# Kernel tuning notes

Measured on AMD Instinct MI355X. Metric: run time of the kernel, lower is better.

## Reference

```python
import jax, jax.numpy as jnp
import numpy as np

N = 20000      # nodes
E = 320000     # edges
F = 32         # node_feat_dim
H = 128        # hidden_dim
HEADS = 4
DH = 128       # out_channels per head (PyG TransformerConv semantics)
L = 2          # number of GNNBlocks actually built


def _ln(x, s, b, eps=1e-5):
    m = x.mean(-1, keepdims=True)
    v = ((x - m) ** 2).mean(-1, keepdims=True)
    return (x - m) / jnp.sqrt(v + eps) * s + b


def setup_inputs() -> dict:
    key = jax.random.key(0)
    ks = jax.random.split(key, 16)
    nrm = lambda k, sh, sc=0.05: jax.random.normal(k, sh, dtype=jnp.float32) * sc
    inp = {}
    inp['x'] = jax.random.normal(ks[0], (N, F), dtype=jnp.float32)
    inp['edge_index'] = jax.random.randint(ks[1], (2, E), 0, N)
    inp['Win'] = nrm(ks[2], (F, H))
    inp['b_in'] = jnp.zeros((H,), jnp.float32)
    inp['ln1_s'] = jnp.ones((L, H), jnp.float32)
    inp['ln1_b'] = jnp.zeros((L, H), jnp.float32)
    inp['Wq'] = nrm(ks[3], (L, H, HEADS * DH))
    inp['bq'] = jnp.zeros((L, HEADS * DH), jnp.float32)
    inp['Wk'] = nrm(ks[4], (L, H, HEADS * DH))
    inp['bk'] = jnp.zeros((L, HEADS * DH), jnp.float32)
    inp['Wv'] = nrm(ks[5], (L, H, HEADS * DH))
    inp['bv'] = jnp.zeros((L, HEADS * DH), jnp.float32)
    inp['Wskip'] = nrm(ks[6], (L, H, H))
    inp['bskip'] = jnp.zeros((L, H), jnp.float32)
    inp['Wbeta'] = nrm(ks[7], (L, 3 * H, 1))
    inp['ln2_s'] = jnp.ones((L, H), jnp.float32)
    inp['ln2_b'] = jnp.zeros((L, H), jnp.float32)
    inp['W1'] = nrm(ks[8], (L, H, 4 * H))
    inp['b1'] = jnp.zeros((L, 4 * H), jnp.float32)
    inp['W2'] = nrm(ks[9], (L, 4 * H, H))
    inp['b2'] = jnp.zeros((L, H), jnp.float32)
    inp['g1'] = jnp.ones((L,), jnp.float32)
    inp['g2'] = jnp.ones((L,), jnp.float32)
    inp['lno_s'] = jnp.ones((H,), jnp.float32)
    inp['lno_b'] = jnp.zeros((H,), jnp.float32)
    return inp


def reference(x, edge_index, Win, b_in, ln1_s, ln1_b, Wq, bq, Wk, bk, Wv, bv,
              Wskip, bskip, Wbeta, ln2_s, ln2_b, W1, b1, W2, b2, g1, g2,
              lno_s, lno_b):
    src, dst = edge_index[0], edge_index[1]  # messages flow src -> dst
    n = x.shape[0]
    scale = 1.0 / np.sqrt(DH).astype(np.float32)
    h = x @ Win + b_in  # [N,H]
    for l in range(L):
        # --- pre-norm TransformerConv (heads=4, concat=False, beta=True) ---
        hn = _ln(h, ln1_s[l], ln1_b[l])
        q = (hn @ Wq[l] + bq[l]).reshape(n, HEADS, DH)
        k = (hn @ Wk[l] + bk[l]).reshape(n, HEADS, DH)
        v = (hn @ Wv[l] + bv[l]).reshape(n, HEADS, DH)
        # per-edge attention logits [E, HEADS]
        alpha = jnp.einsum('ehd,ehd->eh', q[dst], k[src]) * scale
        # segment softmax over incoming edges of each target node
        amax = jax.ops.segment_max(alpha, dst, num_segments=n)  # [N,HEADS]
        num = jnp.exp(alpha - amax[dst])
        den = jax.ops.segment_sum(num, dst, num_segments=n)      # [N,HEADS]
        a = num / den[dst]                                       # [E,HEADS]
        # scatter-aggregate weighted values, then mean over heads (concat=False)
        agg = jax.ops.segment_sum(a[:, :, None] * v[src], dst, num_segments=n)
        out = agg.mean(axis=1)                                   # [N,H]
        # root skip + beta gate
        xr = hn @ Wskip[l] + bskip[l]
        beta = jax.nn.sigmoid(
            jnp.concatenate([out, xr, out - xr], axis=-1) @ Wbeta[l])  # [N,1]
        attn = beta * xr + (1.0 - beta) * out
        h = h + g1[l] * attn
        # --- pre-norm FFN ---
        hn2 = _ln(h, ln2_s[l], ln2_b[l])
        ffn = jax.nn.gelu(hn2 @ W1[l] + b1[l], approximate=False) @ W2[l] + b2[l]
        h = h + g2[l] * ffn
    return _ln(h, lno_s, lno_b)
```

## Files before the change

### kernel.cpp

```cpp
#include <hip/hip_runtime.h>
#include <hip/hip_bf16.h>
#include <math.h>

#define NN 20000
#define NE 320000

typedef unsigned short ushort_t;
typedef unsigned short ushortx8 __attribute__((ext_vector_type(8)));
typedef short s16x8 __attribute__((ext_vector_type(8)));
typedef float f32x4 __attribute__((ext_vector_type(4)));
typedef float f32x2 __attribute__((ext_vector_type(2)));

__device__ __forceinline__ float us2f(unsigned short u){
  return __uint_as_float(((unsigned)u) << 16);
}
__device__ __forceinline__ unsigned short f2us(float f){
  unsigned u = __float_as_uint(f);
  unsigned r = (u + 0x7fffu + ((u >> 16) & 1u)) >> 16;
  return (unsigned short)r;
}
__device__ __forceinline__ void e4m3x8_to_f32(uint2 d, float* out){
  f32x2 a = __builtin_amdgcn_cvt_pk_f32_fp8(d.x, false);
  f32x2 b = __builtin_amdgcn_cvt_pk_f32_fp8(d.x, true);
  f32x2 c = __builtin_amdgcn_cvt_pk_f32_fp8(d.y, false);
  f32x2 e = __builtin_amdgcn_cvt_pk_f32_fp8(d.y, true);
  out[0] = a.x; out[1] = a.y; out[2] = b.x; out[3] = b.y;
  out[4] = c.x; out[5] = c.y; out[6] = e.x; out[7] = e.y;
}
__device__ __forceinline__ uint2 f32x8_to_e4m3(const float* f){
  unsigned lo = __builtin_amdgcn_cvt_pk_fp8_f32(f[0], f[1], 0u, false);
  lo = __builtin_amdgcn_cvt_pk_fp8_f32(f[2], f[3], lo, true);
  unsigned hi = __builtin_amdgcn_cvt_pk_fp8_f32(f[4], f[5], 0u, false);
  hi = __builtin_amdgcn_cvt_pk_fp8_f32(f[6], f[7], hi, true);
  return make_uint2(lo, hi);
}

__global__ void k_hist(const int* __restrict__ ei, int* __restrict__ deg){
  int e = blockIdx.x * 256 + threadIdx.x;
  if (e < NE) atomicAdd(&deg[ei[NE + e]], 1);
}

__global__ __launch_bounds__(1024) void k_scan(const int* __restrict__ deg,
                                               int* __restrict__ rowst,
                                               int* __restrict__ cur){
  __shared__ int ws[16];
  int tid = threadIdx.x;
  int lane = tid & 63, wid = tid >> 6;
  int carry = 0;
  for (int base = 0; base < NN; base += 1024){
    int i = base + tid;
    int v = (i < NN) ? deg[i] : 0;
    int incl = v;
    #pragma unroll
    for (int off = 1; off < 64; off <<= 1){
      int t = __shfl_up(incl, off);
      if (lane >= off) incl += t;
    }
    if (lane == 63) ws[wid] = incl;
    __syncthreads();
    int tot = 0, woff = 0;
    #pragma unroll
    for (int k2 = 0; k2 < 16; k2++){
      int wv = ws[k2];
      tot += wv;
      if (k2 < wid) woff += wv;
    }
    int excl = carry + woff + incl - v;
    if (i < NN){ rowst[i] = excl; cur[i] = excl; }
    carry += tot;
    __syncthreads();
  }
  if (tid == 0) rowst[NN] = carry;
}

__global__ void k_scatter(const int* __restrict__ ei, int* __restrict__ cur,
                          int* __restrict__ srcs){
  int e = blockIdx.x * 256 + threadIdx.x;
  if (e < NE){
    int s = ei[e];
    int d = ei[NE + e];
    int p = atomicAdd(&cur[d], 1);
    srcs[p] = s;
  }
}

__global__ void k_wt(const float* __restrict__ Wq, const float* __restrict__ Wk,
                     const float* __restrict__ Wv, const float* __restrict__ Wsk,
                     const float* __restrict__ W1, const float* __restrict__ W2,
                     const float* __restrict__ bq, const float* __restrict__ bk,
                     const float* __restrict__ bv, const float* __restrict__ bsk,
                     ushort_t* __restrict__ out, float* __restrict__ bcat,
                     int* __restrict__ deg){
  int f = blockIdx.x * 256 + threadIdx.x;
  if (f < 688128){
    float val;
    if (f < 425984){
      int l = f / 212992, idx = f % 212992;
      int n = idx / 128, kk = idx % 128;
      if (n < 512)       val = Wq[(size_t)l * 65536 + kk * 512 + n];
      else if (n < 1024) val = Wk[(size_t)l * 65536 + kk * 512 + (n - 512)];
      else if (n < 1536) val = Wv[(size_t)l * 65536 + kk * 512 + (n - 1024)];
      else               val = Wsk[(size_t)l * 16384 + kk * 128 + (n - 1536)];
    } else if (f < 557056){
      int idx = f - 425984;
      int l = idx / 65536, r = idx % 65536;
      int n = r / 128, kk = r % 128;
      val = W1[(size_t)l * 65536 + kk * 512 + n];
    } else {
      int idx = f - 557056;
      int l = idx / 65536, r = idx % 65536;
      int n = r / 512, kk = r % 512;
      val = W2[(size_t)l * 65536 + kk * 128 + n];
    }
    out[f] = f2us(val);
  } else if (f < 691456){
    int i = f - 688128;
    int l = i / 1664, c = i % 1664;
    float v;
    if (c < 512)       v = bq[l * 512 + c];
    else if (c < 1024) v = bk[l * 512 + c - 512];
    else if (c < 1536) v = bv[l * 512 + c - 1024];
    else               v = bsk[l * 128 + c - 1536];
    bcat[i] = v;
  } else if (f < 711456){
    deg[f - 691456] = 0;
  }
}

__global__ __launch_bounds__(128) void k_inproj(const float* __restrict__ x,
                                                const float* __restrict__ Win,
                                                const float* __restrict__ bin,
                                                float* __restrict__ h){
  __shared__ float sW[32 * 128];
  __shared__ float sx[16][32];
  int tid = threadIdx.x;
  for (int i = 0; i < 32; i++) sW[i * 128 + tid] = Win[i * 128 + tid];
  int r0 = blockIdx.x * 16;
  for (int rr = tid >> 5; rr < 16; rr += 4){
    int gr = r0 + rr;
    sx[rr][tid & 31] = (gr < NN) ? x[(size_t)gr * 32 + (tid & 31)] : 0.f;
  }
  __syncthreads();
  float bias = bin[tid];
  for (int r = 0; r < 16; r++){
    int gr = r0 + r;
    if (gr >= NN) break;
    float acc = bias;
    #pragma unroll
    for (int k2 = 0; k2 < 32; k2++) acc += sx[r][k2] * sW[k2 * 128 + tid];
    h[(size_t)gr * 128 + tid] = acc;
  }
}

template<int OUTBF16>
__global__ void k_ln(const float* __restrict__ in, const float* __restrict__ sc,
                     const float* __restrict__ bi, void* __restrict__ outp, int rows){
  int row = blockIdx.x * 4 + (threadIdx.x >> 6);
  int lane = threadIdx.x & 63;
  if (row >= rows) return;
  const float* p = in + (size_t)row * 128 + lane * 2;
  float x0 = p[0], x1 = p[1];
  float sum = x0 + x1;
  for (int m = 1; m < 64; m <<= 1) sum += __shfl_xor(sum, m);
  float mean = sum * (1.f / 128.f);
  float d0 = x0 - mean, d1 = x1 - mean;
  float vs = d0 * d0 + d1 * d1;
  for (int m = 1; m < 64; m <<= 1) vs += __shfl_xor(vs, m);
  float rstd = rsqrtf(vs * (1.f / 128.f) + 1e-5f);
  int d = lane * 2;
  float o0 = d0 * rstd * sc[d] + bi[d];
  float o1 = d1 * rstd * sc[d + 1] + bi[d + 1];
  if (OUTBF16){
    ushort_t* o = (ushort_t*)outp + (size_t)row * 128 + d;
    o[0] = f2us(o0); o[1] = f2us(o1);
  } else {
    float* o = (float*)outp + (size_t)row * 128 + d;
    o[0] = o0; o[1] = o1;
  }
}

template<int MODE>
__global__ __launch_bounds__(256) void k_mm(const ushort_t* __restrict__ A, int M, int K,
                                            const ushort_t* __restrict__ Bt,
                                            const float* __restrict__ bias,
                                            void* __restrict__ Cp, int ldc,
                                            const float* __restrict__ gptr,
                                            ushort_t* __restrict__ qout,
                                            unsigned char* __restrict__ kvout,
                                            ushort_t* __restrict__ xrout,
                                            int nbn){
  __shared__ ushort_t smem[2 * 128 * 72];
  ushort_t* As = smem;
  ushort_t* Bs = smem + 128 * 72;
  int tid = threadIdx.x;
  int nwg = gridDim.x;
  int orig = blockIdx.x;
  int q8 = nwg >> 3, r8 = nwg & 7;
  int xcd = orig & 7, jj = orig >> 3;
  int wgid = (xcd < r8) ? (xcd * (q8 + 1) + jj)
                        : (r8 * (q8 + 1) + (xcd - r8) * q8 + jj);
  int m0 = (wgid / nbn) * 128, n0 = (wgid % nbn) * 128;
  int lane = tid & 63, w = tid >> 6;
  int wm = (w >> 1) * 64, wn = (w & 1) * 64;
  int fr = lane & 15, fq = lane >> 4;
  f32x4 acc[4][4];
  #pragma unroll
  for (int i = 0; i < 4; i++)
    #pragma unroll
    for (int j = 0; j < 4; j++) acc[i][j] = (f32x4){0.f, 0.f, 0.f, 0.f};

  for (int k0 = 0; k0 < K; k0 += 64){
    __syncthreads();
    #pragma unroll
    for (int it = 0; it < 4; it++){
      int idx = it * 256 + tid;
      int row = idx >> 3, ks = (idx & 7) * 8;
      int gr = m0 + row; if (gr >= M) gr = M - 1;
      *(ushortx8*)&As[row * 72 + ks] = *(const ushortx8*)(A + (size_t)gr * K + k0 + ks);
      *(ushortx8*)&Bs[row * 72 + ks] = *(const ushortx8*)(Bt + (size_t)(n0 + row) * K + k0 + ks);
    }
    __syncthreads();
    #pragma unroll
    for (int ks = 0; ks < 64; ks += 32){
      s16x8 a[4], b[4];
      #pragma unroll
      for (int i = 0; i < 4; i++)
        a[i] = *(const s16x8*)&As[(wm + i * 16 + fr) * 72 + ks + fq * 8];
      #pragma unroll
      for (int j = 0; j < 4; j++)
        b[j] = *(const s16x8*)&Bs[(wn + j * 16 + fr) * 72 + ks + fq * 8];
      #pragma unroll
      for (int i = 0; i < 4; i++)
        #pragma unroll
        for (int j = 0; j < 4; j++)
          acc[i][j] = __builtin_amdgcn_mfma_f32_16x16x32_bf16(a[i], b[j], acc[i][j], 0, 0, 0);
    }
  }

  if (MODE == 2){
    float g = *gptr;
    #pragma unroll
    for (int i = 0; i < 4; i++){
      int grb = m0 + wm + i * 16 + fq * 4;
      #pragma unroll
      for (int r = 0; r < 4; r++){
        int gr = grb + r;
        if (gr >= M) continue;
        #pragma unroll
        for (int j = 0; j < 4; j++){
          int gc = n0 + wn + j * 16 + fr;
          float c = acc[i][j][r] + bias[gc];
          ((float*)Cp)[(size_t)gr * ldc + gc] += g * c;
        }
      }
    }
    return;
  }

  __syncthreads();
  ushort_t* Cs = smem;
  #pragma unroll
  for (int i = 0; i < 4; i++){
    int rowb = wm + i * 16 + fq * 4;
    #pragma unroll
    for (int j = 0; j < 4; j++){
      int col = wn + j * 16 + fr;
      float bv = bias[n0 + col];
      #pragma unroll
      for (int r = 0; r < 4; r++){
        float c = acc[i][j][r] + bv;
        if (MODE == 1) c = 0.5f * c * (1.f + erff(c * 0.70710678118654752f));
        Cs[(rowb + r) * 136 + col] = f2us(c);
      }
    }
  }
  __syncthreads();
  #pragma unroll
  for (int it = 0; it < 8; it++){
    int idx = it * 256 + tid;
    int row = idx >> 4, seg = idx & 15;
    int gr = m0 + row;
    if (gr >= M) continue;
    ushortx8 cv = *(const ushortx8*)&Cs[row * 136 + seg * 8];
    int gc = n0 + seg * 8;
    if (MODE == 1){
      *(ushortx8*)((ushort_t*)Cp + (size_t)gr * ldc + gc) = cv;
    } else {
      if (n0 < 512){
        *(ushortx8*)(qout + (size_t)gr * 512 + gc) = cv;
      } else if (n0 < 1536){
        float fv[8];
        #pragma unroll
        for (int t = 0; t < 8; t++) fv[t] = us2f(cv[t]);
        uint2 pk = f32x8_to_e4m3(fv);
        if (n0 < 1024){
          *(uint2*)(kvout + (size_t)gr * 1024 + (size_t)((gc - 512) >> 3) * 16) = pk;
        } else {
          *(uint2*)(kvout + (size_t)gr * 1024 + (size_t)((gc - 1024) >> 3) * 16 + 8) = pk;
        }
      } else {
        *(ushortx8*)(xrout + (size_t)gr * 128 + (gc - 1536)) = cv;
      }
    }
  }
}

__global__ void k_attn(const ushort_t* __restrict__ q, const unsigned char* __restrict__ kv8,
                       const int* __restrict__ rowst, const int* __restrict__ srcs,
                       const ushort_t* __restrict__ xr, const float* __restrict__ Wb,
                       const float* __restrict__ g1p, float* __restrict__ h,
                       const float* __restrict__ sc2, const float* __restrict__ bi2,
                       ushort_t* __restrict__ hn){
  int n = blockIdx.x * 4 + (threadIdx.x >> 6);
  int lane = threadIdx.x & 63;
  if (n >= NN) return;
  int s0 = rowst[n], s1 = rowst[n + 1];
  int deg = s1 - s0;
  float qf[8];
  {
    ushortx8 qv = *((const ushortx8*)(q + (size_t)n * 512) + lane);
    #pragma unroll
    for (int t = 0; t < 8; t++) qf[t] = us2f(qv[t]);
  }
  const float scale = 0.08838834764831845f;
  const uint4* kvb = (const uint4*)kv8;
  float l = 0.f;
  float acc[8] = {0.f, 0.f, 0.f, 0.f, 0.f, 0.f, 0.f, 0.f};
  for (int c0 = s0; c0 < s1; c0 += 64){
    int rem = s1 - c0; if (rem > 64) rem = 64;
    int se = (lane < rem) ? srcs[c0 + lane] : 0;
    int j = 0;
    for (; j + 8 <= rem; j += 8){
      uint4 kvd[8];
      #pragma unroll
      for (int u = 0; u < 8; u++){
        int sv = __builtin_amdgcn_readlane(se, j + u);
        kvd[u] = kvb[(size_t)sv * 64 + lane];
      }
      #pragma unroll
      for (int u = 0; u < 8; u++){
        float kf[8];
        e4m3x8_to_f32(make_uint2(kvd[u].x, kvd[u].y), kf);
        float p = 0.f;
        #pragma unroll
        for (int t = 0; t < 8; t++) p += qf[t] * kf[t];
        p += __shfl_xor(p, 1); p += __shfl_xor(p, 2);
        p += __shfl_xor(p, 4); p += __shfl_xor(p, 8);
        float w = __expf(p * scale);
        float vf[8];
        e4m3x8_to_f32(make_uint2(kvd[u].z, kvd[u].w), vf);
        l += w;
        #pragma unroll
        for (int t = 0; t < 8; t++) acc[t] += w * vf[t];
      }
    }
    for (; j + 4 <= rem; j += 4){
      uint4 kvd[4];
      #pragma unroll
      for (int u = 0; u < 4; u++){
        int sv = __builtin_amdgcn_readlane(se, j + u);
        kvd[u] = kvb[(size_t)sv * 64 + lane];
      }
      #pragma unroll
      for (int u = 0; u < 4; u++){
        float kf[8];
        e4m3x8_to_f32(make_uint2(kvd[u].x, kvd[u].y), kf);
        float p = 0.f;
        #pragma unroll
        for (int t = 0; t < 8; t++) p += qf[t] * kf[t];
        p += __shfl_xor(p, 1); p += __shfl_xor(p, 2);
        p += __shfl_xor(p, 4); p += __shfl_xor(p, 8);
        float w = __expf(p * scale);
        float vf[8];
        e4m3x8_to_f32(make_uint2(kvd[u].z, kvd[u].w), vf);
        l += w;
        #pragma unroll
        for (int t = 0; t < 8; t++) acc[t] += w * vf[t];
      }
    }
    for (; j < rem; j++){
      int sv0 = __builtin_amdgcn_readlane(se, j);
      uint4 kvd = kvb[(size_t)sv0 * 64 + lane];
      float kf[8];
      e4m3x8_to_f32(make_uint2(kvd.x, kvd.y), kf);
      float p0 = 0.f;
      #pragma unroll
      for (int t = 0; t < 8; t++) p0 += qf[t] * kf[t];
      p0 += __shfl_xor(p0, 1); p0 += __shfl_xor(p0, 2);
      p0 += __shfl_xor(p0, 4); p0 += __shfl_xor(p0, 8);
      float w = __expf(p0 * scale);
      float vf[8];
      e4m3x8_to_f32(make_uint2(kvd.z, kvd.w), vf);
      l += w;
      #pragma unroll
      for (int t = 0; t < 8; t++) acc[t] += w * vf[t];
    }
  }
  float inv = deg ? (0.25f / l) : 0.f;
  #pragma unroll
  for (int t = 0; t < 8; t++){
    float r = acc[t] * inv;
    r += __shfl_xor(r, 16); r += __shfl_xor(r, 32);
    acc[t] = r;
  }
  if (lane < 16){
    int d = lane * 8;
    float xv[8];
    {
      ushortx8 xrv = *(const ushortx8*)(xr + (size_t)n * 128 + d);
      #pragma unroll
      for (int t = 0; t < 8; t++) xv[t] = us2f(xrv[t]);
    }
    float pp = 0.f;
    #pragma unroll
    for (int t = 0; t < 8; t++){
      float w0 = Wb[d + t], w1 = Wb[128 + d + t], w2 = Wb[256 + d + t];
      pp += acc[t] * (w0 + w2) + xv[t] * (w1 - w2);
    }
    pp += __shfl_xor(pp, 1); pp += __shfl_xor(pp, 2);
    pp += __shfl_xor(pp, 4); pp += __shfl_xor(pp, 8);
    float beta = 1.f / (1.f + __expf(-pp));
    float g = *g1p;
    float* hp = h + (size_t)n * 128 + d;
    float hv[8];
    {
      float4 h0 = *(const float4*)(hp);
      float4 h1 = *(const float4*)(hp + 4);
      hv[0]=h0.x; hv[1]=h0.y; hv[2]=h0.z; hv[3]=h0.w;
      hv[4]=h1.x; hv[5]=h1.y; hv[6]=h1.z; hv[7]=h1.w;
    }
    #pragma unroll
    for (int t = 0; t < 8; t++)
      hv[t] += g * (beta * xv[t] + (1.f - beta) * acc[t]);
    float s = 0.f;
    #pragma unroll
    for (int t = 0; t < 8; t++) s += hv[t];
    s += __shfl_xor(s, 1); s += __shfl_xor(s, 2);
    s += __shfl_xor(s, 4); s += __shfl_xor(s, 8);
    float mean = s * (1.f / 128.f);
    float vs = 0.f;
    #pragma unroll
    for (int t = 0; t < 8; t++){ float dd = hv[t] - mean; vs += dd * dd; }
    vs += __shfl_xor(vs, 1); vs += __shfl_xor(vs, 2);
    vs += __shfl_xor(vs, 4); vs += __shfl_xor(vs, 8);
    float rstd = rsqrtf(vs * (1.f / 128.f) + 1e-5f);
    *(float4*)(hp) = make_float4(hv[0], hv[1], hv[2], hv[3]);
    *(float4*)(hp + 4) = make_float4(hv[4], hv[5], hv[6], hv[7]);
    ushortx8 hno;
    #pragma unroll
    for (int t = 0; t < 8; t++)
      hno[t] = f2us((hv[t] - mean) * rstd * sc2[d + t] + bi2[d + t]);
    *(ushortx8*)(hn + (size_t)n * 128 + d) = hno;
  }
}

extern "C" void kernel_launch(void* const* d_in, const int* in_sizes, int n_in,
                              void* d_out, int out_size, void* d_ws, size_t ws_size,
                              hipStream_t stream){
  const float* x    = (const float*)d_in[0];
  const int*   ei   = (const int*)d_in[1];
  const float* Win  = (const float*)d_in[2];
  const float* bin  = (const float*)d_in[3];
  const float* ln1s = (const float*)d_in[4];
  const float* ln1b = (const float*)d_in[5];
  const float* Wq   = (const float*)d_in[6];
  const float* bq   = (const float*)d_in[7];
  const float* Wk   = (const float*)d_in[8];
  const float* bk   = (const float*)d_in[9];
  const float* Wv   = (const float*)d_in[10];
  const float* bv   = (const float*)d_in[11];
  const float* Wsk  = (const float*)d_in[12];
  const float* bsk  = (const float*)d_in[13];
  const float* Wbt  = (const float*)d_in[14];
  const float* ln2s = (const float*)d_in[15];
  const float* ln2b = (const float*)d_in[16];
  const float* W1   = (const float*)d_in[17];
  const float* b1   = (const float*)d_in[18];
  const float* W2   = (const float*)d_in[19];
  const float* b2   = (const float*)d_in[20];
  const float* g1   = (const float*)d_in[21];
  const float* g2   = (const float*)d_in[22];
  const float* lnos = (const float*)d_in[23];
  const float* lnob = (const float*)d_in[24];

  char* wsb = (char*)d_ws;
  size_t off = 0;
  float*         h    = (float*)(wsb + off);         off += (size_t)NN * 128 * 4;
  ushort_t*      hn   = (ushort_t*)(wsb + off);      off += (size_t)NN * 128 * 2;
  ushort_t*      qbuf = (ushort_t*)(wsb + off);      off += (size_t)NN * 512 * 2;
  unsigned char* kv8  = (unsigned char*)(wsb + off); off += (size_t)NN * 1024;
  ushort_t*      xrb  = (ushort_t*)(wsb + off);      off += (size_t)NN * 128 * 2;
  ushort_t*      tb   = (ushort_t*)(wsb + off);      off += (size_t)NN * 512 * 2;
  ushort_t*      wt   = (ushort_t*)(wsb + off);      off += (size_t)688128 * 2;
  float*         bcat = (float*)(wsb + off);         off += (size_t)3328 * 4;
  int*           deg   = (int*)(wsb + off);          off += (size_t)NN * 4;
  int*           rowst = (int*)(wsb + off);          off += (size_t)(NN + 4) * 4;
  int*           cur   = (int*)(wsb + off);          off += (size_t)NN * 4;
  int*           srcs  = (int*)(wsb + off);          off += (size_t)NE * 4;
  ushort_t* Wcat = wt;
  ushort_t* W1t  = wt + 425984;
  ushort_t* W2t  = wt + 557056;

  k_wt<<<2780, 256, 0, stream>>>(Wq, Wk, Wv, Wsk, W1, W2, bq, bk, bv, bsk, wt, bcat, deg);
  k_hist<<<(NE + 255) / 256, 256, 0, stream>>>(ei, deg);
  k_scan<<<1, 1024, 0, stream>>>(deg, rowst, cur);
  k_scatter<<<(NE + 255) / 256, 256, 0, stream>>>(ei, cur, srcs);
  k_inproj<<<(NN + 15) / 16, 128, 0, stream>>>(x, Win, bin, h);

  for (int l = 0; l < 2; l++){
    k_ln<1><<<(NN + 3) / 4, 256, 0, stream>>>(h, ln1s + l * 128, ln1b + l * 128, hn, NN);
    k_mm<3><<<157 * 13, 256, 0, stream>>>(hn, NN, 128, Wcat + (size_t)l * 212992, bcat + l * 1664,
                                          nullptr, 0, nullptr, qbuf, kv8, xrb, 13);
    k_attn<<<(NN + 3) / 4, 256, 0, stream>>>(qbuf, kv8, rowst, srcs, xrb, Wbt + l * 384,
                                             g1 + l, h, ln2s + l * 128, ln2b + l * 128, hn);
    k_mm<1><<<157 * 4, 256, 0, stream>>>(hn, NN, 128, W1t + (size_t)l * 65536, b1 + l * 512,
                                         tb, 512, nullptr, nullptr, nullptr, nullptr, 4);
    k_mm<2><<<157, 256, 0, stream>>>(tb, NN, 512, W2t + (size_t)l * 65536, b2 + l * 128,
                                     h, 128, g2 + l, nullptr, nullptr, nullptr, 1);
  }
  k_ln<0><<<(NN + 3) / 4, 256, 0, stream>>>(h, lnos, lnob, (float*)d_out, NN);
}
```

Before: 434.4 us.

## Fuse layernorms into producer kernels, single-pass scan, DPP reductions, double-buffered edge loads

Removes the standalone layernorm kernels by folding LN1 into the input projection and LN1/final-LN into the W2 GEMM epilogue, where the block re-reads its just-written rows after a block barrier. Replaces the looped single-block scan with a per-thread serial scan of 20 elements, swaps shuffle-based 16-lane reductions for DPP adds, and double-buffers the gathered K/V loads in the attention kernel to overlap memory with compute. This cuts launches and global round trips but adds a serial LN tail per GEMM block and relies on the block writing complete 128-wide rows.

After: 497.0 us. 14.4% more time.

```diff
diff --git a/kernel.cpp b/kernel.cpp
--- a/kernel.cpp
+++ b/kernel.cpp
@@ -34,6 +34,18 @@
   hi = __builtin_amdgcn_cvt_pk_fp8_f32(f[6], f[7], hi, true);
   return make_uint2(lo, hi);
 }
+template<int CTRL>
+__device__ __forceinline__ float dpp_add(float x){
+  int t = __builtin_amdgcn_update_dpp(0, __float_as_int(x), CTRL, 0xf, 0xf, true);
+  return x + __int_as_float(t);
+}
+__device__ __forceinline__ float red16(float p){
+  p = dpp_add<0xB1>(p);
+  p = dpp_add<0x4E>(p);
+  p = dpp_add<0x141>(p);
+  p = dpp_add<0x140>(p);
+  return p;
+}
 
 __global__ void k_hist(const int* __restrict__ ei, int* __restrict__ deg){
   int e = blockIdx.x * 256 + threadIdx.x;
@@ -46,31 +58,34 @@
   __shared__ int ws[16];
   int tid = threadIdx.x;
   int lane = tid & 63, wid = tid >> 6;
-  int carry = 0;
-  for (int base = 0; base < NN; base += 1024){
-    int i = base + tid;
-    int v = (i < NN) ? deg[i] : 0;
-    int incl = v;
-    #pragma unroll
-    for (int off = 1; off < 64; off <<= 1){
-      int t = __shfl_up(incl, off);
-      if (lane >= off) incl += t;
-    }
-    if (lane == 63) ws[wid] = incl;
-    __syncthreads();
-    int tot = 0, woff = 0;
-    #pragma unroll
-    for (int k2 = 0; k2 < 16; k2++){
-      int wv = ws[k2];
-      tot += wv;
-      if (k2 < wid) woff += wv;
-    }
-    int excl = carry + woff + incl - v;
-    if (i < NN){ rowst[i] = excl; cur[i] = excl; }
-    carry += tot;
-    __syncthreads();
-  }
-  if (tid == 0) rowst[NN] = carry;
+  int base = tid * 20;
+  int v[20];
+  int s = 0;
+  #pragma unroll
+  for (int u = 0; u < 20; u++){
+    int i = base + u;
+    int d = (i < NN) ? deg[i] : 0;
+    v[u] = s;
+    s += d;
+  }
+  int incl = s;
+  #pragma unroll
+  for (int off = 1; off < 64; off <<= 1){
+    int t = __shfl_up(incl, off);
+    if (lane >= off) incl += t;
+  }
+  if (lane == 63) ws[wid] = incl;
+  __syncthreads();
+  int woff = 0;
+  #pragma unroll
+  for (int k2 = 0; k2 < 16; k2++) if (k2 < wid) woff += ws[k2];
+  int toff = woff + incl - s;
+  #pragma unroll
+  for (int u = 0; u < 20; u++){
+    int i = base + u;
+    if (i < NN){ int e = toff + v[u]; rowst[i] = e; cur[i] = e; }
+  }
+  if (tid == 1023) rowst[NN] = toff + s;
 }
 
 __global__ void k_scatter(const int* __restrict__ ei, int* __restrict__ cur,
@@ -130,7 +145,10 @@
 __global__ __launch_bounds__(128) void k_inproj(const float* __restrict__ x,
                                                 const float* __restrict__ Win,
                                                 const float* __restrict__ bin,
-                                                float* __restrict__ h){
+                                                float* __restrict__ h,
+                                                const float* __restrict__ sc,
+                                                const float* __restrict__ bi,
+                                                ushort_t* __restrict__ hn){
   __shared__ float sW[32 * 128];
   __shared__ float sx[16][32];
   int tid = threadIdx.x;
@@ -150,32 +168,26 @@
     for (int k2 = 0; k2 < 32; k2++) acc += sx[r][k2] * sW[k2 * 128 + tid];
     h[(size_t)gr * 128 + tid] = acc;
   }
-}
-
-template<int OUTBF16>
-__global__ void k_ln(const float* __restrict__ in, const float* __restrict__ sc,
-                     const float* __restrict__ bi, void* __restrict__ outp, int rows){
-  int row = blockIdx.x * 4 + (threadIdx.x >> 6);
-  int lane = threadIdx.x & 63;
-  if (row >= rows) return;
-  const float* p = in + (size_t)row * 128 + lane * 2;
-  float x0 = p[0], x1 = p[1];
-  float sum = x0 + x1;
-  for (int m = 1; m < 64; m <<= 1) sum += __shfl_xor(sum, m);
-  float mean = sum * (1.f / 128.f);
-  float d0 = x0 - mean, d1 = x1 - mean;
-  float vs = d0 * d0 + d1 * d1;
-  for (int m = 1; m < 64; m <<= 1) vs += __shfl_xor(vs, m);
-  float rstd = rsqrtf(vs * (1.f / 128.f) + 1e-5f);
-  int d = lane * 2;
-  float o0 = d0 * rstd * sc[d] + bi[d];
-  float o1 = d1 * rstd * sc[d + 1] + bi[d + 1];
-  if (OUTBF16){
-    ushort_t* o = (ushort_t*)outp + (size_t)row * 128 + d;
-    o[0] = f2us(o0); o[1] = f2us(o1);
-  } else {
-    float* o = (float*)outp + (size_t)row * 128 + d;
-    o[0] = o0; o[1] = o1;
+  __threadfence_block();
+  __syncthreads();
+  int lane = tid & 63, wv = tid >> 6;
+  for (int rr = 0; rr < 8; rr++){
+    int r = wv * 8 + rr;
+    int gr = r0 + r;
+    if (gr >= NN) continue;
+    const float* p = h + (size_t)gr * 128 + lane * 2;
+    float x0 = p[0], x1 = p[1];
+    float sum = x0 + x1;
+    for (int m = 1; m < 64; m <<= 1) sum += __shfl_xor(sum, m);
+    float mean = sum * (1.f / 128.f);
+    float d0 = x0 - mean, d1 = x1 - mean;
+    float vs = d0 * d0 + d1 * d1;
+    for (int m = 1; m < 64; m <<= 1) vs += __shfl_xor(vs, m);
+    float rstd = rsqrtf(vs * (1.f / 128.f) + 1e-5f);
+    int d = lane * 2;
+    ushort_t* o = hn + (size_t)gr * 128 + d;
+    o[0] = f2us(d0 * rstd * sc[d] + bi[d]);
+    o[1] = f2us(d1 * rstd * sc[d + 1] + bi[d + 1]);
   }
 }
 
@@ -188,7 +200,10 @@
                                             ushort_t* __restrict__ qout,
                                             unsigned char* __restrict__ kvout,
                                             ushort_t* __restrict__ xrout,
-                                            int nbn){
+                                            int nbn,
+                                            const float* __restrict__ lns,
+                                            const float* __restrict__ lnb,
+                                            void* __restrict__ lnout){
   __shared__ ushort_t smem[2 * 128 * 72];
   ushort_t* As = smem;
   ushort_t* Bs = smem + 128 * 72;
@@ -237,7 +252,7 @@
     }
   }
 
-  if (MODE == 2){
+  if (MODE == 2 || MODE == 5){
     float g = *gptr;
     #pragma unroll
     for (int i = 0; i < 4; i++){
@@ -250,8 +265,36 @@
         for (int j = 0; j < 4; j++){
           int gc = n0 + wn + j * 16 + fr;
           float c = acc[i][j][r] + bias[gc];
-          ((float*)Cp)[(size_t)gr * ldc + gc] += g * c;
+          float* hp = (float*)Cp + (size_t)gr * ldc + gc;
+          *hp = *hp + g * c;
         }
+      }
+    }
+    __threadfence_block();
+    __syncthreads();
+    int w4 = tid >> 6;
+    for (int rr = 0; rr < 32; rr++){
+      int row = w4 * 32 + rr;
+      int gr = m0 + row;
+      if (gr >= M) continue;
+      const float* p = (const float*)Cp + (size_t)gr * ldc + lane * 2;
+      float x0 = p[0], x1 = p[1];
+      float sum = x0 + x1;
+      for (int m = 1; m < 64; m <<= 1) sum += __shfl_xor(sum, m);
+      float mean = sum * (1.f / 128.f);
+      float d0 = x0 - mean, d1 = x1 - mean;
+      float vs = d0 * d0 + d1 * d1;
+      for (int m = 1; m < 64; m <<= 1) vs += __shfl_xor(vs, m);
+      float rstd = rsqrtf(vs * (1.f / 128.f) + 1e-5f);
+      int d = lane * 2;
+      float o0 = d0 * rstd * lns[d] + lnb[d];
+      float o1 = d1 * rstd * lns[d + 1] + lnb[d + 1];
+      if (MODE == 2){
+        ushort_t* o = (ushort_t*)lnout + (size_t)gr * 128 + d;
+        o[0] = f2us(o0); o[1] = f2us(o1);
+      } else {
+        float* o = (float*)lnout + (size_t)gr * 128 + d;
+        o[0] = o0; o[1] = o1;
       }
     }
     return;
@@ -305,6 +348,19 @@
   }
 }
 
+#define EDGE_PROC(KVD) {                                                     \
+    float kf[8]; e4m3x8_to_f32(make_uint2((KVD).x, (KVD).y), kf);            \
+    float p = 0.f;                                                           \
+    _Pragma("unroll")                                                        \
+    for (int t = 0; t < 8; t++) p += qf[t] * kf[t];                          \
+    p = red16(p);                                                            \
+    float wgt = __expf(p * scale);                                           \
+    float vf[8]; e4m3x8_to_f32(make_uint2((KVD).z, (KVD).w), vf);            \
+    l += wgt;                                                                \
+    _Pragma("unroll")                                                        \
+    for (int t = 0; t < 8; t++) acc[t] += wgt * vf[t];                       \
+  }
+
 __global__ void k_attn(const ushort_t* __restrict__ q, const unsigned char* __restrict__ kv8,
                        const int* __restrict__ rowst, const int* __restrict__ srcs,
                        const ushort_t* __restrict__ xr, const float* __restrict__ Wb,
@@ -329,71 +385,33 @@
   for (int c0 = s0; c0 < s1; c0 += 64){
     int rem = s1 - c0; if (rem > 64) rem = 64;
     int se = (lane < rem) ? srcs[c0 + lane] : 0;
-    int j = 0;
-    for (; j + 8 <= rem; j += 8){
-      uint4 kvd[8];
-      #pragma unroll
-      for (int u = 0; u < 8; u++){
-        int sv = __builtin_amdgcn_readlane(se, j + u);
-        kvd[u] = kvb[(size_t)sv * 64 + lane];
-      }
-      #pragma unroll
-      for (int u = 0; u < 8; u++){
-        float kf[8];
-        e4m3x8_to_f32(make_uint2(kvd[u].x, kvd[u].y), kf);
-        float p = 0.f;
-        #pragma unroll
-        for (int t = 0; t < 8; t++) p += qf[t] * kf[t];
-        p += __shfl_xor(p, 1); p += __shfl_xor(p, 2);
-        p += __shfl_xor(p, 4); p += __shfl_xor(p, 8);
-        float w = __expf(p * scale);
-        float vf[8];
-        e4m3x8_to_f32(make_uint2(kvd[u].z, kvd[u].w), vf);
-        l += w;
-        #pragma unroll
-        for (int t = 0; t < 8; t++) acc[t] += w * vf[t];
-      }
-    }
-    for (; j + 4 <= rem; j += 4){
-      uint4 kvd[4];
-      #pragma unroll
-      for (int u = 0; u < 4; u++){
-        int sv = __builtin_amdgcn_readlane(se, j + u);
-        kvd[u] = kvb[(size_t)sv * 64 + lane];
-      }
-      #pragma unroll
-      for (int u = 0; u < 4; u++){
-        float kf[8];
-        e4m3x8_to_f32(make_uint2(kvd[u].x, kvd[u].y), kf);
-        float p = 0.f;
-        #pragma unroll
-        for (int t = 0; t < 8; t++) p += qf[t] * kf[t];
-        p += __shfl_xor(p, 1); p += __shfl_xor(p, 2);
-        p += __shfl_xor(p, 4); p += __shfl_xor(p, 8);
-        float w = __expf(p * scale);
-        float vf[8];
-        e4m3x8_to_f32(make_uint2(kvd[u].z, kvd[u].w), vf);
-        l += w;
-        #pragma unroll
-        for (int t = 0; t < 8; t++) acc[t] += w * vf[t];
-      }
-    }
-    for (; j < rem; j++){
-      int sv0 = __builtin_amdgcn_readlane(se, j);
-      uint4 kvd = kvb[(size_t)sv0 * 64 + lane];
-      float kf[8];
-      e4m3x8_to_f32(make_uint2(kvd.x, kvd.y), kf);
-      float p0 = 0.f;
-      #pragma unroll
-      for (int t = 0; t < 8; t++) p0 += qf[t] * kf[t];
-      p0 += __shfl_xor(p0, 1); p0 += __shfl_xor(p0, 2);
-      p0 += __shfl_xor(p0, 4); p0 += __shfl_xor(p0, 8);
-      float w = __expf(p0 * scale);
-      float vf[8];
-      e4m3x8_to_f32(make_uint2(kvd.z, kvd.w), vf);
-      l += w;
-      #pragma unroll
-      for (int t = 0; t < 8; t++) acc[t] += w * vf[t];
+    uint4 bufA[8], bufB[8];
+    int jA = 0;
+    int cA = rem < 8 ? rem : 8;
+    #pragma unroll
+    for (int u = 0; u < 8; u++)
+      if (u < cA)
+        bufA[u] = kvb[(size_t)__builtin_amdgcn_readlane(se, u) * 64 + lane];
+    while (jA < rem){
+      int jB = jA + cA;
+      int cB = rem - jB; cB = cB < 0 ? 0 : (cB > 8 ? 8 : cB);
+      #pragma unroll
+      for (int u = 0; u < 8; u++)
+        if (u < cB)
+          bufB[u] = kvb[(size_t)__builtin_amdgcn_readlane(se, jB + u) * 64 + lane];
+      #pragma unroll
+      for (int u = 0; u < 8; u++)
+        if (u < cA) EDGE_PROC(bufA[u]);
+      int jA2 = jB + cB;
+      int cA2 = rem - jA2; cA2 = cA2 < 0 ? 0 : (cA2 > 8 ? 8 : cA2);
+      #pragma unroll
+      for (int u = 0; u < 8; u++)
+        if (u < cA2)
+          bufA[u] = kvb[(size_t)__builtin_amdgcn_readlane(se, jA2 + u) * 64 + lane];
+      #pragma unroll
+      for (int u = 0; u < 8; u++)
+        if (u < cB) EDGE_PROC(bufB[u]);
+      jA = jA2; cA = cA2;
     }
   }
   float inv = deg ? (0.25f / l) : 0.f;
@@ -417,8 +435,7 @@
       float w0 = Wb[d + t], w1 = Wb[128 + d + t], w2 = Wb[256 + d + t];
       pp += acc[t] * (w0 + w2) + xv[t] * (w1 - w2);
     }
-    pp += __shfl_xor(pp, 1); pp += __shfl_xor(pp, 2);
-    pp += __shfl_xor(pp, 4); pp += __shfl_xor(pp, 8);
+    pp = red16(pp);
     float beta = 1.f / (1.f + __expf(-pp));
     float g = *g1p;
     float* hp = h + (size_t)n * 128 + d;
@@ -435,14 +452,12 @@
     float s = 0.f;
     #pragma unroll
     for (int t = 0; t < 8; t++) s += hv[t];
-    s += __shfl_xor(s, 1); s += __shfl_xor(s, 2);
-    s += __shfl_xor(s, 4); s += __shfl_xor(s, 8);
+    s = red16(s);
     float mean = s * (1.f / 128.f);
     float vs = 0.f;
     #pragma unroll
     for (int t = 0; t < 8; t++){ float dd = hv[t] - mean; vs += dd * dd; }
-    vs += __shfl_xor(vs, 1); vs += __shfl_xor(vs, 2);
-    vs += __shfl_xor(vs, 4); vs += __shfl_xor(vs, 8);
+    vs = red16(vs);
     float rstd = rsqrtf(vs * (1.f / 128.f) + 1e-5f);
     *(float4*)(hp) = make_float4(hv[0], hv[1], hv[2], hv[3]);
     *(float4*)(hp + 4) = make_float4(hv[4], hv[5], hv[6], hv[7]);
@@ -505,18 +520,25 @@
   k_hist<<<(NE + 255) / 256, 256, 0, stream>>>(ei, deg);
   k_scan<<<1, 1024, 0, stream>>>(deg, rowst, cur);
   k_scatter<<<(NE + 255) / 256, 256, 0, stream>>>(ei, cur, srcs);
-  k_inproj<<<(NN + 15) / 16, 128, 0, stream>>>(x, Win, bin, h);
+  k_inproj<<<NN / 16, 128, 0, stream>>>(x, Win, bin, h, ln1s, ln1b, hn);
 
   for (int l = 0; l < 2; l++){
-    k_ln<1><<<(NN + 3) / 4, 256, 0, stream>>>(h, ln1s + l * 128, ln1b + l * 128, hn, NN);
     k_mm<3><<<157 * 13, 256, 0, stream>>>(hn, NN, 128, Wcat + (size_t)l * 212992, bcat + l * 1664,
-                                          nullptr, 0, nullptr, qbuf, kv8, xrb, 13);
+                                          nullptr, 0, nullptr, qbuf, kv8, xrb, 13,
+                                          nullptr, nullptr, nullptr);
     k_attn<<<(NN + 3) / 4, 256, 0, stream>>>(qbuf, kv8, rowst, srcs, xrb, Wbt + l * 384,
                                              g1 + l, h, ln2s + l * 128, ln2b + l * 128, hn);
     k_mm<1><<<157 * 4, 256, 0, stream>>>(hn, NN, 128, W1t + (size_t)l * 65536, b1 + l * 512,
-                                         tb, 512, nullptr, nullptr, nullptr, nullptr, 4);
-    k_mm<2><<<157, 256, 0, stream>>>(tb, NN, 512, W2t + (size_t)l * 65536, b2 + l * 128,
-                                     h, 128, g2 + l, nullptr, nullptr, nullptr, 1);
-  }
-  k_ln<0><<<(NN + 3) / 4, 256, 0, stream>>>(h, lnos, lnob, (float*)d_out, NN);
-}
+                                         tb, 512, nullptr, nullptr, nullptr, nullptr, 4,
+                                         nullptr, nullptr, nullptr);
+    if (l == 0){
+      k_mm<2><<<157, 256, 0, stream>>>(tb, NN, 512, W2t, b2, h, 128, g2,
+                                       nullptr, nullptr, nullptr, 1,
+                                       ln1s + 128, ln1b + 128, hn);
+    } else {
+      k_mm<5><<<157, 256, 0, stream>>>(tb, NN, 512, W2t + 65536, b2 + 128, h, 128, g2 + 1,
+                                       nullptr, nullptr, nullptr, 1,
+                                       lnos, lnob, d_out);
+    }
+  }
+}
```
